# Performance work log

Hardware: AMD Instinct MI355X
Metric: run time of the kernel (lower is better)

Reference implementation:

```python
import jax, jax.numpy as jnp
import numpy as np
from jax import lax

B, CIN, H, W = 8, 64, 128, 128
COUT, K, STRIDE, PAD = 128, 3, 1, 1
NLEV = 256  # 2**activation_bits == 2**weight_bits


def setup_inputs() -> dict:
    key = jax.random.key(0)
    kx, kw = jax.random.split(key)
    x = jax.random.uniform(kx, (B, CIN, H, W), dtype=jnp.float32)
    weight = jax.random.normal(kw, (COUT, CIN, K, K), dtype=jnp.float32)
    bias = jnp.zeros((COUT,), dtype=jnp.float32)
    return {"x": x, "weight": weight, "bias": bias}


def _lut_table(weight):
    # quantized weights in [0, 255], integer-valued
    qw = jnp.clip(jnp.round(weight * (NLEV - 1)), 0, NLEV - 1).astype(jnp.int32)
    iv = jnp.arange(NLEV, dtype=jnp.int32)
    # emulate torch .to(int16) wraparound (qw*i can exceed 32767)
    lut = (qw[..., None] * iv).astype(jnp.int16)          # [O, C, K, K, 256]
    # the original sums pcilt over its (c,p,q) dims for EVERY patch entry;
    # precollapse those dims: T[i, o] = sum_{c,p,q} lut[o,c,p,q,i]
    T = lut.astype(jnp.int32).sum(axis=(1, 2, 3))          # [O, 256]
    return T.T                                             # [256, O]


def reference(x, weight, bias):
    T = _lut_table(weight)                                 # [256, COUT]
    xq = jnp.clip(jnp.round(x * (NLEV - 1)), 0, NLEV - 1).astype(jnp.int32)
    xp = jnp.pad(xq, ((0, 0), (0, 0), (PAD, PAD), (PAD, PAD)))  # zero-pad; T[:,0]=0 matches
    xc = jnp.moveaxis(xp, 1, 0)                            # [CIN, B, Hp, Wp]

    # accumulate per-pixel channel sum of LUT rows: A[b,h,w,o] = sum_c T[x[b,c,h,w], o]
    A0 = jnp.zeros((xp.shape[0], xp.shape[2], xp.shape[3], COUT), dtype=jnp.int32)

    def body(acc, ch):
        return acc + T[ch], None

    A, _ = lax.scan(body, A0, xc)                          # [B, Hp, Wp, COUT]

    # k x k sliding-window sum over spatial dims = sum over all patch entries
    out = lax.reduce_window(A.astype(jnp.float32), 0.0, lax.add,
                            (1, K, K, 1), (1, STRIDE, STRIDE, 1), 'VALID')
    out = jnp.moveaxis(out, 3, 1) + bias[None, :, None, None]  # [B, COUT, OH, OW]
    return out
```

## Files before the change

kernel.cpp:

```cpp
#include <hip/hip_runtime.h>

#define CIN   64
#define HW    128
#define COUT  128
#define TH    8
#define TW    32
#define PXR   34
#define NITER (TH + 2)
#define NTHR  512
#define HSTR  144
#define AKSTR 136

typedef int v4i __attribute__((ext_vector_type(4)));

__global__ __launch_bounds__(128)
void build_tables(const float* __restrict__ weight, int* __restrict__ W_tab,
                  char* __restrict__ Kt_g) {
  __shared__ int qw_s[576];
  __shared__ int red_s[128];
  const int o = blockIdx.x;
  const int t = threadIdx.x;
  int partial = 0;
  for (int j = t; j < 576; j += 128) {
    float w = weight[o * 576 + j];
    int q = (int)rintf(w * 255.f);
    q = q < 0 ? 0 : (q > 255 ? 255 : q);
    qw_s[j] = q;
    partial += q;
  }
  red_s[t] = partial;
  __syncthreads();
  for (int s = 64; s > 0; s >>= 1) {
    if (t < s) red_s[t] += red_s[t + s];
    __syncthreads();
  }
  if (t == 0) W_tab[o] = red_s[0];
  const int i = 128 + t;
  int cnt = 0;
  for (int j = 0; j < 576; ++j) cnt += (qw_s[j] * i) > 32767 ? 1 : 0;
  Kt_g[o * 128 + t] = (char)(cnt - 128);
}

__global__ __launch_bounds__(NTHR, 4)
void pcilt_main(const float* __restrict__ x, const float* __restrict__ bias,
                const int* __restrict__ W_tab, const char* __restrict__ Kt_g,
                float* __restrict__ out) {
  __shared__ unsigned char Hm[4][48 * HSTR];
  __shared__ unsigned char Kt[128 * 128];
  __shared__ unsigned short AK[48 * AKSTR];
  __shared__ int Sxr[4][PXR];
  __shared__ int SHr[4][PXR];

  const int t   = (int)threadIdx.x;
  const int bid = (int)blockIdx.x;
  const int b  = bid & 7;
  const int k  = bid >> 3;
  const int h0 = (k >> 2) * TH;
  const int w0 = (k & 3) * TW;

  for (int i = t; i < 128 * 128 / 4; i += NTHR)
    ((unsigned int*)Kt)[i] = ((const unsigned int*)Kt_g)[i];
  for (int i = t; i < 48 * HSTR / 4; i += NTHR)
    ((unsigned int*)Hm[0])[i] = 0u;

  const int l    = t & 15;
  const int slot = t >> 4;
  const int w    = t >> 6;
  const int kq   = (t >> 4) & 3;
  const int we   = t & 31;
  const int og   = t >> 5;

  float wf[8], bi[8];
#pragma unroll
  for (int m = 0; m < 8; ++m) {
    wf[m] = (float)W_tab[og * 8 + m];
    bi[m] = bias[og * 8 + m];
  }

  __syncthreads();

  v4i bfr[4][2];
  const int Mt = w >> 1, Nh = w & 1;
  if (w < 6) {
#pragma unroll
    for (int nt = 0; nt < 4; ++nt)
#pragma unroll
      for (int k64 = 0; k64 < 2; ++k64)
        bfr[nt][k64] = *(const v4i*)(Kt + (Nh * 64 + nt * 16 + l) * 128 +
                                     k64 * 64 + kq * 16);
  }

  float pf0[4], pf1[4];
  const float* xb = x + ((size_t)b * CIN + l * 4) * (HW * HW);
  const size_t cs = (size_t)HW * HW;

#define ISSUE(rn)                                                              \
  {                                                                            \
    const int iy  = h0 + (rn)-1;                                               \
    const int iyc = iy < 0 ? 0 : (iy > 127 ? 127 : iy);                        \
    const bool rok = (iy >= 0) && (iy < HW);                                   \
    int ix = w0 + slot - 1;                                                    \
    int ixc = ix < 0 ? 0 : (ix > 127 ? 127 : ix);                              \
    bool ok = rok && (ix >= 0) && (ix < HW);                                   \
    const float* xp = xb + (size_t)iyc * HW + ixc;                             \
    float v0 = xp[0], v1 = xp[cs], v2 = xp[2 * cs], v3 = xp[3 * cs];           \
    pf0[0] = ok ? v0 : 0.f; pf0[1] = ok ? v1 : 0.f;                            \
    pf0[2] = ok ? v2 : 0.f; pf0[3] = ok ? v3 : 0.f;                            \
    if (slot < 2) {                                                            \
      ix = w0 + 32 + slot - 1;                                                 \
      ixc = ix > 127 ? 127 : ix;                                               \
      ok = rok && (ix < HW);                                                   \
      const float* xq = xb + (size_t)iyc * HW + ixc;                           \
      float u0 = xq[0], u1 = xq[cs], u2 = xq[2 * cs], u3 = xq[3 * cs];         \
      pf1[0] = ok ? u0 : 0.f; pf1[1] = ok ? u1 : 0.f;                          \
      pf1[2] = ok ? u2 : 0.f; pf1[3] = ok ? u3 : 0.f;                          \
    }                                                                          \
  }

#define STAGEPX(pf, px)                                                        \
  {                                                                            \
    int q, iv0, iv1, iv2, iv3;                                                 \
    q = (int)rintf((pf)[0] * 255.f); iv0 = q < 0 ? 0 : (q > 255 ? 255 : q);    \
    q = (int)rintf((pf)[1] * 255.f); iv1 = q < 0 ? 0 : (q > 255 ? 255 : q);    \
    q = (int)rintf((pf)[2] * 255.f); iv2 = q < 0 ? 0 : (q > 255 ? 255 : q);    \
    q = (int)rintf((pf)[3] * 255.f); iv3 = q < 0 ? 0 : (q > 255 ? 255 : q);    \
    int ps = iv0 + iv1 + iv2 + iv3;                                            \
    int pc = (iv0 > 128) + (iv1 > 128) + (iv2 > 128) + (iv3 > 128);            \
    ps += __shfl_xor(ps, 1, 16); pc += __shfl_xor(pc, 1, 16);                  \
    ps += __shfl_xor(ps, 2, 16); pc += __shfl_xor(pc, 2, 16);                  \
    ps += __shfl_xor(ps, 4, 16); pc += __shfl_xor(pc, 4, 16);                  \
    ps += __shfl_xor(ps, 8, 16); pc += __shfl_xor(pc, 8, 16);                  \
    if (l == 0) { Sxr[r & 3][px] = ps; SHr[r & 3][px] = pc; }                  \
    unsigned char* hp = Hc + (px)*HSTR;                                        \
    if (iv0 > 128) { int v = iv0 - 128; atomicAdd((unsigned int*)(hp + ((v >> 2) << 2)), 1u << ((v & 3) * 8)); } \
    if (iv1 > 128) { int v = iv1 - 128; atomicAdd((unsigned int*)(hp + ((v >> 2) << 2)), 1u << ((v & 3) * 8)); } \
    if (iv2 > 128) { int v = iv2 - 128; atomicAdd((unsigned int*)(hp + ((v >> 2) << 2)), 1u << ((v & 3) * 8)); } \
    if (iv3 > 128) { int v = iv3 - 128; atomicAdd((unsigned int*)(hp + ((v >> 2) << 2)), 1u << ((v & 3) * 8)); } \
  }

  ISSUE(0);

  for (int r = 0; r < NITER; ++r) {
    {
      unsigned char* Hc = (unsigned char*)Hm[r & 3];
      STAGEPX(pf0, slot);
      if (slot < 2) STAGEPX(pf1, 32 + slot);
    }
    if (r + 1 < NITER) ISSUE(r + 1);
    __syncthreads();

    if (r >= 2 && w < 6) {
      v4i acc[4];
#pragma unroll
      for (int nt = 0; nt < 4; ++nt) acc[nt] = (v4i){0, 0, 0, 0};
      const int prow = Mt * 16 + (t & 15);
#pragma unroll
      for (int st = 0; st < 3; ++st) {
        const unsigned char* Hs = (const unsigned char*)Hm[(r - 2 + st) & 3] +
                                  prow * HSTR + kq * 16;
#pragma unroll
        for (int k64 = 0; k64 < 2; ++k64) {
          const v4i a = *(const v4i*)(Hs + k64 * 64);
#pragma unroll
          for (int nt = 0; nt < 4; ++nt)
            acc[nt] = __builtin_amdgcn_mfma_i32_16x16x64_i8(a, bfr[nt][k64], acc[nt], 0, 0, 0);
        }
      }
      const int pbase = Mt * 16 + kq * 4;
#pragma unroll
      for (int nt = 0; nt < 4; ++nt) {
        const int o = Nh * 64 + nt * 16 + (t & 15);
#pragma unroll
        for (int rg = 0; rg < 4; ++rg)
          AK[(pbase + rg) * AKSTR + o] = (unsigned short)acc[nt][rg];
      }
    }
    if (w >= 6) {
      uint4* Hn = (uint4*)Hm[(r + 1) & 3];
      const uint4 z4 = make_uint4(0, 0, 0, 0);
      for (int i = t - 384; i < 48 * HSTR / 16; i += 128) Hn[i] = z4;
    }
    __syncthreads();

    if (r >= 2) {
      const int h = h0 + r - 2;
      int sx9 = 0, sh9 = 0;
#pragma unroll
      for (int q = 0; q < 3; ++q) {
        const int sl = (r - 2 + q) & 3;
        sx9 += Sxr[sl][we] + Sxr[sl][we + 1] + Sxr[sl][we + 2];
        sh9 += SHr[sl][we] + SHr[sl][we + 1] + SHr[sl][we + 2];
      }
      int k0 = 0, k1 = 0, k2 = 0, k3 = 0, k4 = 0, k5 = 0, k6 = 0, k7 = 0;
#pragma unroll
      for (int dx = 0; dx < 3; ++dx) {
        const uint4 p = *(const uint4*)&AK[(we + dx) * AKSTR + og * 8];
        k0 += (int)(short)(p.x & 0xffffu); k1 += (int)(short)(p.x >> 16);
        k2 += (int)(short)(p.y & 0xffffu); k3 += (int)(short)(p.y >> 16);
        k4 += (int)(short)(p.z & 0xffffu); k5 += (int)(short)(p.z >> 16);
        k6 += (int)(short)(p.w & 0xffffu); k7 += (int)(short)(p.w >> 16);
      }
      const int kc = 128 * sh9;
      const float sxf = (float)sx9;
      float* op = out + (((size_t)b * COUT + og * 8) * HW + h) * HW + (w0 + we);
      const size_t os = (size_t)HW * HW;
      op[0 * os] = sxf * wf[0] - 65536.f * (float)(k0 + kc) + bi[0];
      op[1 * os] = sxf * wf[1] - 65536.f * (float)(k1 + kc) + bi[1];
      op[2 * os] = sxf * wf[2] - 65536.f * (float)(k2 + kc) + bi[2];
      op[3 * os] = sxf * wf[3] - 65536.f * (float)(k3 + kc) + bi[3];
      op[4 * os] = sxf * wf[4] - 65536.f * (float)(k4 + kc) + bi[4];
      op[5 * os] = sxf * wf[5] - 65536.f * (float)(k5 + kc) + bi[5];
      op[6 * os] = sxf * wf[6] - 65536.f * (float)(k6 + kc) + bi[6];
      op[7 * os] = sxf * wf[7] - 65536.f * (float)(k7 + kc) + bi[7];
    }
  }
}

extern "C" void kernel_launch(void* const* d_in, const int* in_sizes, int n_in,
                              void* d_out, int out_size, void* d_ws, size_t ws_size,
                              hipStream_t stream) {
  const float* x      = (const float*)d_in[0];
  const float* weight = (const float*)d_in[1];
  const float* bias   = (const float*)d_in[2];
  float* out = (float*)d_out;

  int*  W_tab = (int*)d_ws;
  char* Kt_g  = (char*)d_ws + 512;

  build_tables<<<128, 128, 0, stream>>>(weight, W_tab, Kt_g);

  pcilt_main<<<512, NTHR, 0, stream>>>(x, bias, W_tab, Kt_g, out);
}
```

Measured before the change: 47.38 us.

## Software-pipeline histogram, MFMA and epilogue stages with one barrier per row

Restructures the row loop so the MFMA stage and the output epilogue run one iteration apart, using a 5-deep histogram ring, double-buffered AK and an 8-slot sum ring. This removes one of the two workgroup barriers per iteration. The per-pixel shuffle reduction of the pixel sum and high-count is replaced by a single packed LDS atomicAdd (count in bits 20+, sum in the low 20 bits). A custom barrier that waits only on lgkmcnt is also added. The cost is an extra loop iteration, more LDS use (which may lower occupancy), and more LDS atomic contention.

```diff
diff --git a/kernel.cpp b/kernel.cpp
--- a/kernel.cpp
+++ b/kernel.cpp
@@ -6,12 +6,16 @@
 #define TH    8
 #define TW    32
 #define PXR   34
-#define NITER (TH + 2)
+#define NITER (TH + 3)
 #define NTHR  512
 #define HSTR  144
 #define AKSTR 136
 
 typedef int v4i __attribute__((ext_vector_type(4)));
+
+__device__ __forceinline__ void wg_barrier() {
+  asm volatile("s_waitcnt lgkmcnt(0)\n\ts_barrier" ::: "memory");
+}
 
 __global__ __launch_bounds__(128)
 void build_tables(const float* __restrict__ weight, int* __restrict__ W_tab,
@@ -45,11 +49,10 @@
 void pcilt_main(const float* __restrict__ x, const float* __restrict__ bias,
                 const int* __restrict__ W_tab, const char* __restrict__ Kt_g,
                 float* __restrict__ out) {
-  __shared__ unsigned char Hm[4][48 * HSTR];
-  __shared__ unsigned char Kt[128 * 128];
-  __shared__ unsigned short AK[48 * AKSTR];
-  __shared__ int Sxr[4][PXR];
-  __shared__ int SHr[4][PXR];
+  __shared__ unsigned char Hm[5][48 * HSTR];
+  __shared__ unsigned char Kt[16384];
+  __shared__ unsigned short AK[2][48 * AKSTR];
+  __shared__ int SxSH[8][40];
 
   const int t   = (int)threadIdx.x;
   const int bid = (int)blockIdx.x;
@@ -58,10 +61,13 @@
   const int h0 = (k >> 2) * TH;
   const int w0 = (k & 3) * TW;
 
-  for (int i = t; i < 128 * 128 / 4; i += NTHR)
+  for (int i = t; i < 4096; i += NTHR)
     ((unsigned int*)Kt)[i] = ((const unsigned int*)Kt_g)[i];
-  for (int i = t; i < 48 * HSTR / 4; i += NTHR)
-    ((unsigned int*)Hm[0])[i] = 0u;
+  {
+    const uint4 z4 = make_uint4(0, 0, 0, 0);
+    for (int i = t; i < 5 * 48 * HSTR / 16; i += NTHR) ((uint4*)Hm)[i] = z4;
+    if (t < 320) ((int*)SxSH)[t] = 0;
+  }
 
   const int l    = t & 15;
   const int slot = t >> 4;
@@ -77,7 +83,7 @@
     bi[m] = bias[og * 8 + m];
   }
 
-  __syncthreads();
+  wg_barrier();
 
   v4i bfr[4][2];
   const int Mt = w >> 1, Nh = w & 1;
@@ -126,11 +132,7 @@
     q = (int)rintf((pf)[3] * 255.f); iv3 = q < 0 ? 0 : (q > 255 ? 255 : q);    \
     int ps = iv0 + iv1 + iv2 + iv3;                                            \
     int pc = (iv0 > 128) + (iv1 > 128) + (iv2 > 128) + (iv3 > 128);            \
-    ps += __shfl_xor(ps, 1, 16); pc += __shfl_xor(pc, 1, 16);                  \
-    ps += __shfl_xor(ps, 2, 16); pc += __shfl_xor(pc, 2, 16);                  \
-    ps += __shfl_xor(ps, 4, 16); pc += __shfl_xor(pc, 4, 16);                  \
-    ps += __shfl_xor(ps, 8, 16); pc += __shfl_xor(pc, 8, 16);                  \
-    if (l == 0) { Sxr[r & 3][px] = ps; SHr[r & 3][px] = pc; }                  \
+    atomicAdd(&Sp[px], (pc << 20) + ps);                                       \
     unsigned char* hp = Hc + (px)*HSTR;                                        \
     if (iv0 > 128) { int v = iv0 - 128; atomicAdd((unsigned int*)(hp + ((v >> 2) << 2)), 1u << ((v & 3) * 8)); } \
     if (iv1 > 128) { int v = iv1 - 128; atomicAdd((unsigned int*)(hp + ((v >> 2) << 2)), 1u << ((v & 3) * 8)); } \
@@ -141,22 +143,23 @@
   ISSUE(0);
 
   for (int r = 0; r < NITER; ++r) {
-    {
-      unsigned char* Hc = (unsigned char*)Hm[r & 3];
+    if (r <= TH + 1) {
+      unsigned char* Hc = (unsigned char*)Hm[r % 5];
+      int* Sp = SxSH[r & 7];
       STAGEPX(pf0, slot);
       if (slot < 2) STAGEPX(pf1, 32 + slot);
-    }
-    if (r + 1 < NITER) ISSUE(r + 1);
-    __syncthreads();
-
-    if (r >= 2 && w < 6) {
+      if (r + 1 <= TH + 1) ISSUE(r + 1);
+    }
+    wg_barrier();
+
+    if (r >= 2 && r <= TH + 1 && w < 6) {
       v4i acc[4];
 #pragma unroll
       for (int nt = 0; nt < 4; ++nt) acc[nt] = (v4i){0, 0, 0, 0};
       const int prow = Mt * 16 + (t & 15);
 #pragma unroll
       for (int st = 0; st < 3; ++st) {
-        const unsigned char* Hs = (const unsigned char*)Hm[(r - 2 + st) & 3] +
+        const unsigned char* Hs = (const unsigned char*)Hm[(r - 2 + st) % 5] +
                                   prow * HSTR + kq * 16;
 #pragma unroll
         for (int k64 = 0; k64 < 2; ++k64) {
@@ -166,35 +169,38 @@
             acc[nt] = __builtin_amdgcn_mfma_i32_16x16x64_i8(a, bfr[nt][k64], acc[nt], 0, 0, 0);
         }
       }
+      unsigned short* AKw = AK[r & 1];
       const int pbase = Mt * 16 + kq * 4;
 #pragma unroll
       for (int nt = 0; nt < 4; ++nt) {
         const int o = Nh * 64 + nt * 16 + (t & 15);
 #pragma unroll
         for (int rg = 0; rg < 4; ++rg)
-          AK[(pbase + rg) * AKSTR + o] = (unsigned short)acc[nt][rg];
-      }
-    }
-    if (w >= 6) {
-      uint4* Hn = (uint4*)Hm[(r + 1) & 3];
+          AKw[(pbase + rg) * AKSTR + o] = (unsigned short)acc[nt][rg];
+      }
+    }
+    if (w >= 6 && r >= 3 && r <= TH - 1) {
       const uint4 z4 = make_uint4(0, 0, 0, 0);
-      for (int i = t - 384; i < 48 * HSTR / 16; i += 128) Hn[i] = z4;
-    }
-    __syncthreads();
-
-    if (r >= 2) {
-      const int h = h0 + r - 2;
-      int sx9 = 0, sh9 = 0;
+      uint4* Hn = (uint4*)Hm[(r + 2) % 5];
+      for (int i = t - 384; i < 34 * HSTR / 16; i += 128) Hn[i] = z4;
+      if (t - 384 < 40) SxSH[(r + 2) & 7][t - 384] = 0;
+    }
+
+    if (r >= 3) {
+      const int h = h0 + r - 3;
+      const unsigned short* AKr = AK[(r - 1) & 1];
+      int v9 = 0;
 #pragma unroll
       for (int q = 0; q < 3; ++q) {
-        const int sl = (r - 2 + q) & 3;
-        sx9 += Sxr[sl][we] + Sxr[sl][we + 1] + Sxr[sl][we + 2];
-        sh9 += SHr[sl][we] + SHr[sl][we + 1] + SHr[sl][we + 2];
-      }
+        const int sl = (r - 3 + q) & 7;
+        v9 += SxSH[sl][we] + SxSH[sl][we + 1] + SxSH[sl][we + 2];
+      }
+      const int sx9 = v9 & 0xFFFFF;
+      const int sh9 = v9 >> 20;
       int k0 = 0, k1 = 0, k2 = 0, k3 = 0, k4 = 0, k5 = 0, k6 = 0, k7 = 0;
 #pragma unroll
       for (int dx = 0; dx < 3; ++dx) {
-        const uint4 p = *(const uint4*)&AK[(we + dx) * AKSTR + og * 8];
+        const uint4 p = *(const uint4*)&AKr[(we + dx) * AKSTR + og * 8];
         k0 += (int)(short)(p.x & 0xffffu); k1 += (int)(short)(p.x >> 16);
         k2 += (int)(short)(p.y & 0xffffu); k3 += (int)(short)(p.y >> 16);
         k4 += (int)(short)(p.z & 0xffffu); k5 += (int)(short)(p.z >> 16);
```

Result: no change. 46.52 us (-1.8%).
